# Kernel optimization log

Measured on AMD Instinct MI355X. Metric: run time of the kernel, lower is better.

Reference implementation:

```python
import jax, jax.numpy as jnp
import numpy as np

EMBED_DIM = 1024
NUM_HEADS = 16
HEAD_DIM = EMBED_DIM // NUM_HEADS
B, SQ, SKV = 2, 2048, 2048


def setup_inputs() -> dict:
    key = jax.random.key(0)
    ks = jax.random.split(key, 12)
    s = 1.0 / np.sqrt(EMBED_DIM)
    inp = {
        "query": jax.random.normal(ks[0], (B, SQ, EMBED_DIM), jnp.float32),
        "key": jax.random.normal(ks[1], (B, SKV, EMBED_DIM), jnp.float32),
        "value": jax.random.normal(ks[2], (B, SKV, EMBED_DIM), jnp.float32),
        "Wq": jax.random.normal(ks[3], (EMBED_DIM, EMBED_DIM), jnp.float32) * s,
        "bq": jnp.zeros((EMBED_DIM,), jnp.float32),
        "Wk": jax.random.normal(ks[4], (EMBED_DIM, EMBED_DIM), jnp.float32) * s,
        "bk": jnp.zeros((EMBED_DIM,), jnp.float32),
        "Wv": jax.random.normal(ks[5], (EMBED_DIM, EMBED_DIM), jnp.float32) * s,
        "bv": jnp.zeros((EMBED_DIM,), jnp.float32),
        "Wo": jax.random.normal(ks[6], (EMBED_DIM, EMBED_DIM), jnp.float32) * s,
        "bo": jnp.zeros((EMBED_DIM,), jnp.float32),
        "ln_gamma": jnp.ones((EMBED_DIM,), jnp.float32),
        "ln_beta": jnp.zeros((EMBED_DIM,), jnp.float32),
    }
    return inp


def reference(query, key, value, Wq, bq, Wk, bk, Wv, bv, Wo, bo, ln_gamma, ln_beta):
    b, sq, d = query.shape
    skv = key.shape[1]
    residual = query
    # projections -> [b, h, s, hd]
    Q = (query @ Wq + bq).reshape(b, sq, NUM_HEADS, HEAD_DIM).transpose(0, 2, 1, 3)
    K = (key @ Wk + bk).reshape(b, skv, NUM_HEADS, HEAD_DIM).transpose(0, 2, 1, 3)
    V = (value @ Wv + bv).reshape(b, skv, NUM_HEADS, HEAD_DIM).transpose(0, 2, 1, 3)
    scores = jnp.einsum("bhqd,bhkd->bhqk", Q, K) / jnp.sqrt(jnp.float32(HEAD_DIM)).astype(Q.dtype)
    attn = jax.nn.softmax(scores, axis=-1)  # dropout identity in eval
    attended = jnp.einsum("bhqk,bhkd->bhqd", attn, V)
    attended = attended.transpose(0, 2, 1, 3).reshape(b, sq, d)
    out = attended @ Wo + bo
    x = out + residual
    mu = jnp.mean(x, axis=-1, keepdims=True)
    var = jnp.var(x, axis=-1, keepdims=True)
    return (x - mu) / jnp.sqrt(var + 1e-5) * ln_gamma + ln_beta
```

## Files before the change

### kernel.cpp

```cpp
#include <hip/hip_runtime.h>

#define EMBED 1024
#define NHEAD 16
#define HDIM  64
#define BATCH 2
#define SEQ   2048
#define ROWS  (BATCH*SEQ)

typedef __bf16 bf16x8 __attribute__((ext_vector_type(8)));
typedef float  f32x4  __attribute__((ext_vector_type(4)));
typedef float  f32x16 __attribute__((ext_vector_type(16)));
typedef unsigned short u16x8 __attribute__((ext_vector_type(8)));
typedef unsigned short u16x4 __attribute__((ext_vector_type(4)));
typedef unsigned int   u32x2 __attribute__((ext_vector_type(2)));

__device__ __forceinline__ unsigned short f2bf(float f) {
    unsigned int u = __float_as_uint(f);
    u += 0x7FFFu + ((u >> 16) & 1u);
    return (unsigned short)(u >> 16);
}
__device__ __forceinline__ f32x4 zero4() { f32x4 z = {0.f, 0.f, 0.f, 0.f}; return z; }

__device__ __forceinline__ unsigned int cvtpk_bf16(float lo, float hi) {
    unsigned int r;
    asm("v_cvt_pk_bf16_f32 %0, %1, %2" : "=v"(r) : "v"(lo), "v"(hi));
    return r;
}
__device__ __forceinline__ void pl32swap(unsigned int &a, unsigned int &b) {
    asm("v_permlane32_swap_b32 %0, %1" : "+v"(a), "+v"(b));
}
__device__ __forceinline__ float exp2_hw(float x) {
    float r;
    asm("v_exp_f32 %0, %1" : "=v"(r) : "v"(x));
    return r;
}

__device__ __forceinline__ void gl_lds16(const unsigned short* g, unsigned short* l) {
    __builtin_amdgcn_global_load_lds(
        (const __attribute__((address_space(1))) void*)g,
        (__attribute__((address_space(3))) void*)l, 16, 0, 0);
}

__global__ __launch_bounds__(256) void cvt3_kernel(const float* __restrict__ q,
                                                   const float* __restrict__ k,
                                                   const float* __restrict__ v,
                                                   unsigned short* __restrict__ qo,
                                                   unsigned short* __restrict__ ko,
                                                   unsigned short* __restrict__ vo) {
    const float* in; unsigned short* out;
    if (blockIdx.y == 0)      { in = q; out = qo; }
    else if (blockIdx.y == 1) { in = k; out = ko; }
    else                      { in = v; out = vo; }
    int i = (blockIdx.x * 256 + threadIdx.x) * 4;
    float4 vv = *(const float4*)(in + i);
    u16x4 o = {f2bf(vv.x), f2bf(vv.y), f2bf(vv.z), f2bf(vv.w)};
    *(u16x4*)(out + i) = o;
}

__global__ __launch_bounds__(256) void transpose4_kernel(const float* __restrict__ w0,
                                                         const float* __restrict__ w1,
                                                         const float* __restrict__ w2,
                                                         const float* __restrict__ w3,
                                                         unsigned short* __restrict__ o0,
                                                         unsigned short* __restrict__ o1,
                                                         unsigned short* __restrict__ o2,
                                                         unsigned short* __restrict__ o3) {
    const float* in; unsigned short* out;
    if (blockIdx.z == 0)      { in = w0; out = o0; }
    else if (blockIdx.z == 1) { in = w1; out = o1; }
    else if (blockIdx.z == 2) { in = w2; out = o2; }
    else                      { in = w3; out = o3; }
    __shared__ float tile[32][33];
    int tx = threadIdx.x, ty = threadIdx.y;
    int x = blockIdx.x * 32 + tx;
    int y0 = blockIdx.y * 32 + ty;
#pragma unroll
    for (int r = 0; r < 4; ++r)
        tile[ty + 8 * r][tx] = in[(size_t)(y0 + 8 * r) * EMBED + x];
    __syncthreads();
    int ox = blockIdx.y * 32 + tx;
    int oy = blockIdx.x * 32 + ty;
#pragma unroll
    for (int r = 0; r < 4; ++r)
        out[(size_t)(oy + 8 * r) * EMBED + ox] = f2bf(tile[tx][ty + 8 * r]);
}

__global__ __launch_bounds__(256, 2) void gemm_qkv_kernel(
    const unsigned short* __restrict__ qb, const unsigned short* __restrict__ kb,
    const unsigned short* __restrict__ vb,
    const unsigned short* __restrict__ Wqt, const unsigned short* __restrict__ Wkt,
    const unsigned short* __restrict__ Wvt,
    const float* __restrict__ bq, const float* __restrict__ bk, const float* __restrict__ bv,
    unsigned short* __restrict__ Qp, unsigned short* __restrict__ Kp,
    unsigned short* __restrict__ Vtb) {
    __shared__ unsigned short smem[16384];
    const unsigned short *A, *Bt; const float* bias; unsigned short* outp; int mode; float osc;
    if (blockIdx.z == 0)      { A = qb; Bt = Wqt; bias = bq; outp = Qp;  mode = 0; osc = 0.18033688f; }
    else if (blockIdx.z == 1) { A = kb; Bt = Wkt; bias = bk; outp = Kp;  mode = 0; osc = 1.0f; }
    else                      { A = vb; Bt = Wvt; bias = bv; outp = Vtb; mode = 1; osc = 1.0f; }

    const int t = threadIdx.x;
    const int m0 = blockIdx.x * 128, n0 = blockIdx.y * 128;
    const int wave = t >> 6, lane = t & 63;
    const int wr = wave >> 1, wc = wave & 1;
    const int lm = lane & 15, lq = lane >> 4;
    const int sr = t >> 2;
    const int csrc = (t & 3) ^ ((sr >> 1) & 3);
    const int pa = lq ^ ((lm >> 1) & 3);

    const unsigned short* gA = A + (size_t)(m0 + sr) * EMBED + csrc * 8;
    const unsigned short* gB = Bt + (size_t)(n0 + sr) * EMBED + csrc * 8;

    f32x4 acc[4][4];
#pragma unroll
    for (int i = 0; i < 4; ++i)
#pragma unroll
        for (int j = 0; j < 4; ++j) acc[i][j] = zero4();

    gl_lds16(gA,              smem + wave * 512);
    gl_lds16(gA + 64 * EMBED, smem + 2048 + wave * 512);
    gl_lds16(gB,              smem + 8192 + wave * 512);
    gl_lds16(gB + 64 * EMBED, smem + 8192 + 2048 + wave * 512);

    for (int kk = 0; kk < 32; ++kk) {
        __syncthreads();
        if (kk < 31) {
            gA += 32; gB += 32;
            const int nbo = ((kk + 1) & 1) * 4096;
            gl_lds16(gA,              smem + nbo + wave * 512);
            gl_lds16(gA + 64 * EMBED, smem + nbo + 2048 + wave * 512);
            gl_lds16(gB,              smem + 8192 + nbo + wave * 512);
            gl_lds16(gB + 64 * EMBED, smem + 8192 + nbo + 2048 + wave * 512);
        }
        const int cbo = (kk & 1) * 4096;
        bf16x8 af[4], bfr[4];
#pragma unroll
        for (int i = 0; i < 4; ++i)
            af[i] = *(const bf16x8*)&smem[cbo + (wr * 64 + i * 16 + lm) * 32 + pa * 8];
#pragma unroll
        for (int j = 0; j < 4; ++j)
            bfr[j] = *(const bf16x8*)&smem[8192 + cbo + (wc * 64 + j * 16 + lm) * 32 + pa * 8];
#pragma unroll
        for (int i = 0; i < 4; ++i)
#pragma unroll
            for (int j = 0; j < 4; ++j)
                acc[i][j] = __builtin_amdgcn_mfma_f32_16x16x32_bf16(af[i], bfr[j], acc[i][j], 0, 0, 0);
    }

    const int row = t >> 2, seg = t & 3;
    if (mode == 0) {
#pragma unroll
        for (int p = 0; p < 2; ++p) {
            __syncthreads();
            if (wr == p) {
#pragma unroll
                for (int i = 0; i < 4; ++i)
#pragma unroll
                    for (int j = 0; j < 4; ++j) {
                        float bn = bias[n0 + wc * 64 + j * 16 + lm];
                        int nl = wc * 64 + j * 16 + lm;
#pragma unroll
                        for (int r = 0; r < 4; ++r)
                            smem[(i * 16 + lq * 4 + r) * 136 + nl] =
                                f2bf((acc[i][j][r] + bn) * osc);
                    }
            }
            __syncthreads();
            int m = m0 + p * 64 + row;
            int b = m >> 11, sI = m & 2047;
            int ncol = n0 + seg * 32;
            int h = ncol >> 6, hd0 = ncol & 63;
            unsigned short* dst = outp + (((size_t)((b * NHEAD + h) * SEQ + sI)) << 6) + hd0;
            const unsigned short* src = smem + row * 136 + seg * 32;
            *(u16x8*)(dst)      = *(const u16x8*)(src);
            *(u16x8*)(dst + 8)  = *(const u16x8*)(src + 8);
            *(u16x8*)(dst + 16) = *(const u16x8*)(src + 16);
            *(u16x8*)(dst + 24) = *(const u16x8*)(src + 24);
        }
    } else {
#pragma unroll
        for (int p = 0; p < 2; ++p) {
            __syncthreads();
            if (wc == p) {
#pragma unroll
                for (int i = 0; i < 4; ++i)
#pragma unroll
                    for (int j = 0; j < 4; ++j) {
                        float bn = bias[n0 + p * 64 + j * 16 + lm];
                        u16x4 pw = {f2bf(acc[i][j][0] + bn), f2bf(acc[i][j][1] + bn),
                                    f2bf(acc[i][j][2] + bn), f2bf(acc[i][j][3] + bn)};
                        *(u16x4*)&smem[(j * 16 + lm) * 136 + wr * 64 + i * 16 + lq * 4] = pw;
                    }
            }
            __syncthreads();
            int n = n0 + p * 64 + row;
            int h = n >> 6, hd = n & 63;
            int b = m0 >> 11;
            int s0 = (m0 & 2047) + seg * 32;
            unsigned short* dst = outp + ((size_t)((b * NHEAD + h) * HDIM + hd)) * SEQ + s0;
            const unsigned short* src = smem + row * 136 + seg * 32;
            *(u16x8*)(dst)      = *(const u16x8*)(src);
            *(u16x8*)(dst + 8)  = *(const u16x8*)(src + 8);
            *(u16x8*)(dst + 16) = *(const u16x8*)(src + 16);
            *(u16x8*)(dst + 24) = *(const u16x8*)(src + 24);
        }
    }
}

__global__ __launch_bounds__(256, 2) void gemm_o_kernel(
    const unsigned short* __restrict__ att, const unsigned short* __restrict__ Wot,
    const float* __restrict__ bo, float* __restrict__ xbuf,
    const float* __restrict__ residual) {
    __shared__ unsigned short As[2][2048];
    __shared__ unsigned short Bs[2][4096];
    const int t = threadIdx.x;
    const int m0 = blockIdx.x * 64, n0 = blockIdx.y * 128;
    const int wave = t >> 6, lane = t & 63;
    const int lm = lane & 15, lq = lane >> 4;
    const int sr = t >> 2;
    const int csrc = (t & 3) ^ ((sr >> 1) & 3);
    const int pa = lq ^ ((lm >> 1) & 3);

    const unsigned short* gA = att + (size_t)(m0 + sr) * EMBED + csrc * 8;
    const unsigned short* gB = Wot + (size_t)(n0 + sr) * EMBED + csrc * 8;

    f32x4 acc[4][2];
#pragma unroll
    for (int i = 0; i < 4; ++i)
#pragma unroll
        for (int j = 0; j < 2; ++j) acc[i][j] = zero4();

    gl_lds16(gA,              As[0] + wave * 512);
    gl_lds16(gB,              Bs[0] + wave * 512);
    gl_lds16(gB + 64 * EMBED, Bs[0] + 2048 + wave * 512);

    for (int kk = 0; kk < 32; ++kk) {
        __syncthreads();
        if (kk < 31) {
            gA += 32; gB += 32;
            const int nb = (kk + 1) & 1;
            gl_lds16(gA,              As[nb] + wave * 512);
            gl_lds16(gB,              Bs[nb] + wave * 512);
            gl_lds16(gB + 64 * EMBED, Bs[nb] + 2048 + wave * 512);
        }
        const int cb = kk & 1;
        bf16x8 af[4], bfr[2];
#pragma unroll
        for (int i = 0; i < 4; ++i)
            af[i] = *(const bf16x8*)&As[cb][(i * 16 + lm) * 32 + pa * 8];
#pragma unroll
        for (int j = 0; j < 2; ++j)
            bfr[j] = *(const bf16x8*)&Bs[cb][(wave * 32 + j * 16 + lm) * 32 + pa * 8];
#pragma unroll
        for (int i = 0; i < 4; ++i)
#pragma unroll
            for (int j = 0; j < 2; ++j)
                acc[i][j] = __builtin_amdgcn_mfma_f32_16x16x32_bf16(af[i], bfr[j], acc[i][j], 0, 0, 0);
    }

#pragma unroll
    for (int i = 0; i < 4; ++i)
#pragma unroll
        for (int j = 0; j < 2; ++j) {
            int n = n0 + wave * 32 + j * 16 + lm;
            float bn = bo[n];
#pragma unroll
            for (int r = 0; r < 4; ++r) {
                int m = m0 + i * 16 + lq * 4 + r;
                size_t idx = (size_t)m * EMBED + n;
                xbuf[idx] = acc[i][j][r] + bn + residual[idx];
            }
        }
}

__global__ __launch_bounds__(256, 2) void attn_kernel(const unsigned short* __restrict__ Qp,
                                                      const unsigned short* __restrict__ Kp,
                                                      const unsigned short* __restrict__ Vt,
                                                      unsigned short* __restrict__ att) {
    __shared__ unsigned short Ks[16384];
    __shared__ unsigned short Vs[16384];
    const int t = threadIdx.x;
    const int bh = blockIdx.x;
    const int b = bh >> 4, h = bh & 15;
    const int q0 = blockIdx.y * 128;
    const unsigned short* Qh = Qp + (size_t)bh * SEQ * HDIM;
    const unsigned short* Kh = Kp + (size_t)bh * SEQ * HDIM;
    const unsigned short* Vh = Vt + (size_t)bh * HDIM * SEQ;
    const int wave = t >> 6, lane = t & 63;
    const int ln31 = lane & 31, half = lane >> 5;

    bf16x8 qf[4];
    {
        const unsigned short* qptr = Qh + (size_t)(q0 + wave * 32 + ln31) * HDIM + half * 8;
#pragma unroll
        for (int s = 0; s < 4; ++s) qf[s] = *(const bf16x8*)(qptr + s * 16);
    }

    const int q8a = t, q8b = 256 + t;
    const int fa = q8a >> 6, fb = q8b >> 6;
    const int ma = q8a & 31, mb = q8b & 31;
    const int ha = (q8a >> 5) & 1, hb = (q8b >> 5) & 1;
    const unsigned short* gK0 = Kh + (size_t)((fa >> 2) * 32 + ma) * HDIM + (fa & 3) * 16 + ha * 8;
    const unsigned short* gK1 = Kh + (size_t)((fb >> 2) * 32 + mb) * HDIM + (fb & 3) * 16 + hb * 8;
    const unsigned short* gV0 = Vh + (size_t)((fa >> 2) * 32 + ma) * SEQ + (fa & 3) * 16 + ha * 8;
    const unsigned short* gV1 = Vh + (size_t)((fb >> 2) * 32 + mb) * SEQ + (fb & 3) * 16 + hb * 8;

    gl_lds16(gK0,              Ks + wave * 512);
    gl_lds16(gK1,              Ks + 2048 + wave * 512);
    gl_lds16(gK0 + 64 * HDIM,  Ks + 4096 + wave * 512);
    gl_lds16(gK1 + 64 * HDIM,  Ks + 4096 + 2048 + wave * 512);
    gl_lds16(gV0,              Vs + wave * 512);
    gl_lds16(gV1,              Vs + 2048 + wave * 512);
    gl_lds16(gV0 + 64,         Vs + 4096 + wave * 512);
    gl_lds16(gV1 + 64,         Vs + 4096 + 2048 + wave * 512);
    gK0 += 128 * HDIM; gK1 += 128 * HDIM; gV0 += 128; gV1 += 128;
    gl_lds16(gK0,              Ks + 8192 + wave * 512);
    gl_lds16(gK1,              Ks + 8192 + 2048 + wave * 512);
    gl_lds16(gK0 + 64 * HDIM,  Ks + 8192 + 4096 + wave * 512);
    gl_lds16(gK1 + 64 * HDIM,  Ks + 8192 + 4096 + 2048 + wave * 512);
    gl_lds16(gV0,              Vs + 8192 + wave * 512);
    gl_lds16(gV1,              Vs + 8192 + 2048 + wave * 512);
    gl_lds16(gV0 + 64,         Vs + 8192 + 4096 + wave * 512);
    gl_lds16(gV1 + 64,         Vs + 8192 + 4096 + 2048 + wave * 512);
    gK0 += 128 * HDIM; gK1 += 128 * HDIM; gV0 += 128; gV1 += 128;

    f32x16 Oacc[2];
#pragma unroll
    for (int mo = 0; mo < 2; ++mo)
#pragma unroll
        for (int r = 0; r < 16; ++r) Oacc[mo][r] = 0.f;
    float l_run = 0.f;

    for (int kt2 = 0; kt2 < 16; ++kt2) {
        if (kt2 < 15) { asm volatile("s_waitcnt vmcnt(8)" ::: "memory"); }
        else          { asm volatile("s_waitcnt vmcnt(0)" ::: "memory"); }
        __builtin_amdgcn_s_barrier();
        const int cbo = (kt2 & 1) * 8192;

        f32x16 S[2][2];
#pragma unroll
        for (int tl = 0; tl < 2; ++tl)
#pragma unroll
            for (int mt = 0; mt < 2; ++mt)
#pragma unroll
                for (int r = 0; r < 16; ++r) S[tl][mt][r] = -17.312340f;

        __builtin_amdgcn_s_setprio(1);
#pragma unroll
        for (int tl = 0; tl < 2; ++tl)
#pragma unroll
            for (int mt = 0; mt < 2; ++mt) {
#pragma unroll
                for (int s = 0; s < 4; ++s) {
                    bf16x8 af = *(const bf16x8*)&Ks[cbo + tl * 4096 + (mt * 4 + s) * 512 + half * 256 + ln31 * 8];
                    S[tl][mt] = __builtin_amdgcn_mfma_f32_32x32x16_bf16(af, qf[s], S[tl][mt], 0, 0, 0);
                }
            }
        __builtin_amdgcn_s_setprio(0);

#pragma unroll
        for (int tl = 0; tl < 2; ++tl) {
            float rp0 = 0.f, rp1 = 0.f, rp2 = 0.f, rp3 = 0.f;
#pragma unroll
            for (int mt = 0; mt < 2; ++mt)
#pragma unroll
                for (int rg = 0; rg < 4; ++rg) {
                    float p0 = exp2_hw(S[tl][mt][rg * 4 + 0]);
                    float p1 = exp2_hw(S[tl][mt][rg * 4 + 1]);
                    float p2 = exp2_hw(S[tl][mt][rg * 4 + 2]);
                    float p3 = exp2_hw(S[tl][mt][rg * 4 + 3]);
                    S[tl][mt][rg * 4 + 0] = p0; rp0 += p0;
                    S[tl][mt][rg * 4 + 1] = p1; rp1 += p1;
                    S[tl][mt][rg * 4 + 2] = p2; rp2 += p2;
                    S[tl][mt][rg * 4 + 3] = p3; rp3 += p3;
                }
            float rs = (rp0 + rp1) + (rp2 + rp3);
            rs += __shfl_xor(rs, 32);
            l_run += rs;

            __builtin_amdgcn_s_setprio(1);
#pragma unroll
            for (int mt = 0; mt < 2; ++mt)
#pragma unroll
                for (int p = 0; p < 2; ++p) {
                    unsigned int a0 = cvtpk_bf16(S[tl][mt][8 * p + 0], S[tl][mt][8 * p + 1]);
                    unsigned int a1 = cvtpk_bf16(S[tl][mt][8 * p + 2], S[tl][mt][8 * p + 3]);
                    unsigned int b0 = cvtpk_bf16(S[tl][mt][8 * p + 4], S[tl][mt][8 * p + 5]);
                    unsigned int b1 = cvtpk_bf16(S[tl][mt][8 * p + 6], S[tl][mt][8 * p + 7]);
                    pl32swap(a0, b0);
                    pl32swap(a1, b1);
                    union { unsigned int u[4]; bf16x8 v; } bp;
                    bp.u[0] = a0; bp.u[1] = a1; bp.u[2] = b0; bp.u[3] = b1;
                    const int sp = mt * 2 + p;
#pragma unroll
                    for (int mo = 0; mo < 2; ++mo) {
                        bf16x8 av = *(const bf16x8*)&Vs[cbo + tl * 4096 + (mo * 4 + sp) * 512 + half * 256 + ln31 * 8];
                        Oacc[mo] = __builtin_amdgcn_mfma_f32_32x32x16_bf16(av, bp.v, Oacc[mo], 0, 0, 0);
                    }
                }
            __builtin_amdgcn_s_setprio(0);
        }

        if (kt2 < 14) {
            __builtin_amdgcn_s_barrier();
            gl_lds16(gK0,              Ks + cbo + wave * 512);
            gl_lds16(gK1,              Ks + cbo + 2048 + wave * 512);
            gl_lds16(gK0 + 64 * HDIM,  Ks + cbo + 4096 + wave * 512);
            gl_lds16(gK1 + 64 * HDIM,  Ks + cbo + 4096 + 2048 + wave * 512);
            gl_lds16(gV0,              Vs + cbo + wave * 512);
            gl_lds16(gV1,              Vs + cbo + 2048 + wave * 512);
            gl_lds16(gV0 + 64,         Vs + cbo + 4096 + wave * 512);
            gl_lds16(gV1 + 64,         Vs + cbo + 4096 + 2048 + wave * 512);
            gK0 += 128 * HDIM; gK1 += 128 * HDIM; gV0 += 128; gV1 += 128;
        }
    }

    float inv = 1.f / l_run;
    int q = q0 + wave * 32 + ln31;
    unsigned short* orow = att + (size_t)(b * SEQ + q) * EMBED + h * HDIM;
#pragma unroll
    for (int mo = 0; mo < 2; ++mo)
#pragma unroll
        for (int rg = 0; rg < 4; ++rg) {
            u16x4 ow = {f2bf(Oacc[mo][rg * 4 + 0] * inv), f2bf(Oacc[mo][rg * 4 + 1] * inv),
                        f2bf(Oacc[mo][rg * 4 + 2] * inv), f2bf(Oacc[mo][rg * 4 + 3] * inv)};
            *(u16x4*)&orow[mo * 32 + rg * 8 + half * 4] = ow;
        }
}

__global__ __launch_bounds__(256) void ln_kernel(const float* __restrict__ x,
                                                 const float* __restrict__ gamma,
                                                 const float* __restrict__ beta,
                                                 float* __restrict__ out) {
    __shared__ float red[8];
    const int row = blockIdx.x, t = threadIdx.x;
    float4 v = *(const float4*)(x + (size_t)row * EMBED + t * 4);
    float s = v.x + v.y + v.z + v.w;
    float ss = v.x * v.x + v.y * v.y + v.z * v.z + v.w * v.w;
#pragma unroll
    for (int o = 1; o < 64; o <<= 1) {
        s += __shfl_xor(s, o);
        ss += __shfl_xor(ss, o);
    }
    int wave = t >> 6, lane = t & 63;
    if (lane == 0) { red[wave] = s; red[4 + wave] = ss; }
    __syncthreads();
    s = red[0] + red[1] + red[2] + red[3];
    ss = red[4] + red[5] + red[6] + red[7];
    float mu = s * (1.f / EMBED);
    float var = ss * (1.f / EMBED) - mu * mu;
    float rstd = rsqrtf(var + 1e-5f);
    float4 g = *(const float4*)(gamma + t * 4);
    float4 bb = *(const float4*)(beta + t * 4);
    float4 o;
    o.x = (v.x - mu) * rstd * g.x + bb.x;
    o.y = (v.y - mu) * rstd * g.y + bb.y;
    o.z = (v.z - mu) * rstd * g.z + bb.z;
    o.w = (v.w - mu) * rstd * g.w + bb.w;
    *(float4*)(out + (size_t)row * EMBED + t * 4) = o;
}

extern "C" void kernel_launch(void* const* d_in, const int* in_sizes, int n_in,
                              void* d_out, int out_size, void* d_ws, size_t ws_size,
                              hipStream_t stream) {
    const float* query = (const float*)d_in[0];
    const float* key_  = (const float*)d_in[1];
    const float* value = (const float*)d_in[2];
    const float* Wq = (const float*)d_in[3];
    const float* bq = (const float*)d_in[4];
    const float* Wk = (const float*)d_in[5];
    const float* bk = (const float*)d_in[6];
    const float* Wv = (const float*)d_in[7];
    const float* bv = (const float*)d_in[8];
    const float* Wo = (const float*)d_in[9];
    const float* bo = (const float*)d_in[10];
    const float* gamma = (const float*)d_in[11];
    const float* beta  = (const float*)d_in[12];

    char* ws = (char*)d_ws;
    const size_t MB = 1024 * 1024;
    unsigned short* qb  = (unsigned short*)(ws + 0);
    unsigned short* kb  = (unsigned short*)(ws + 8 * MB);
    unsigned short* vb  = (unsigned short*)(ws + 16 * MB);
    unsigned short* Wqt = (unsigned short*)(ws + 24 * MB);
    unsigned short* Wkt = (unsigned short*)(ws + 26 * MB);
    unsigned short* Wvt = (unsigned short*)(ws + 28 * MB);
    unsigned short* Wot = (unsigned short*)(ws + 30 * MB);
    unsigned short* Qp  = (unsigned short*)(ws + 32 * MB);
    unsigned short* Kp  = (unsigned short*)(ws + 40 * MB);
    unsigned short* Vtb = (unsigned short*)(ws + 48 * MB);
    unsigned short* att = (unsigned short*)(ws + 0);
    float*          xbuf = (float*)(ws + 8 * MB);

    cvt3_kernel<<<dim3(4096, 3), 256, 0, stream>>>(query, key_, value, qb, kb, vb);
    transpose4_kernel<<<dim3(32, 32, 4), dim3(32, 8), 0, stream>>>(Wq, Wk, Wv, Wo, Wqt, Wkt, Wvt, Wot);

    gemm_qkv_kernel<<<dim3(32, 8, 3), 256, 0, stream>>>(qb, kb, vb, Wqt, Wkt, Wvt,
                                                        bq, bk, bv, Qp, Kp, Vtb);

    attn_kernel<<<dim3(32, 16), 256, 0, stream>>>(Qp, Kp, Vtb, att);

    gemm_o_kernel<<<dim3(64, 8), 256, 0, stream>>>(att, Wot, bo, xbuf, query);
    ln_kernel<<<ROWS, 256, 0, stream>>>(xbuf, gamma, beta, (float*)d_out);
}
```

Baseline: 247.0 us.

## Deepen GEMM prefetch with vmcnt waits and split attention PV accumulators

Both projection GEMM kernels now prefetch two K-slices up front. Each iteration waits with s_waitcnt vmcnt on only the older slice plus a raw barrier, and the refill of a buffer is issued after its compute, so global loads overlap more of the MFMA work than the previous __syncthreads double buffer did. In the attention kernel the PV output accumulator is split into two independent chains per output tile, summed at the end, to break the MFMA accumulation dependency. The cost is more accumulator registers, which may hurt occupancy, and reliance on hand-tuned vmcnt counts being correct.

```diff
diff --git a/kernel.cpp b/kernel.cpp
--- a/kernel.cpp
+++ b/kernel.cpp
@@ -121,17 +121,17 @@
     gl_lds16(gA + 64 * EMBED, smem + 2048 + wave * 512);
     gl_lds16(gB,              smem + 8192 + wave * 512);
     gl_lds16(gB + 64 * EMBED, smem + 8192 + 2048 + wave * 512);
+    gA += 32; gB += 32;
+    gl_lds16(gA,              smem + 4096 + wave * 512);
+    gl_lds16(gA + 64 * EMBED, smem + 4096 + 2048 + wave * 512);
+    gl_lds16(gB,              smem + 8192 + 4096 + wave * 512);
+    gl_lds16(gB + 64 * EMBED, smem + 8192 + 4096 + 2048 + wave * 512);
+    gA += 32; gB += 32;
 
     for (int kk = 0; kk < 32; ++kk) {
-        __syncthreads();
-        if (kk < 31) {
-            gA += 32; gB += 32;
-            const int nbo = ((kk + 1) & 1) * 4096;
-            gl_lds16(gA,              smem + nbo + wave * 512);
-            gl_lds16(gA + 64 * EMBED, smem + nbo + 2048 + wave * 512);
-            gl_lds16(gB,              smem + 8192 + nbo + wave * 512);
-            gl_lds16(gB + 64 * EMBED, smem + 8192 + nbo + 2048 + wave * 512);
-        }
+        if (kk < 31) { asm volatile("s_waitcnt vmcnt(4)" ::: "memory"); }
+        else         { asm volatile("s_waitcnt vmcnt(0)" ::: "memory"); }
+        __builtin_amdgcn_s_barrier();
         const int cbo = (kk & 1) * 4096;
         bf16x8 af[4], bfr[4];
 #pragma unroll
@@ -145,6 +145,14 @@
 #pragma unroll
             for (int j = 0; j < 4; ++j)
                 acc[i][j] = __builtin_amdgcn_mfma_f32_16x16x32_bf16(af[i], bfr[j], acc[i][j], 0, 0, 0);
+        if (kk < 30) {
+            __builtin_amdgcn_s_barrier();
+            gl_lds16(gA,              smem + cbo + wave * 512);
+            gl_lds16(gA + 64 * EMBED, smem + cbo + 2048 + wave * 512);
+            gl_lds16(gB,              smem + 8192 + cbo + wave * 512);
+            gl_lds16(gB + 64 * EMBED, smem + 8192 + cbo + 2048 + wave * 512);
+            gA += 32; gB += 32;
+        }
     }
 
     const int row = t >> 2, seg = t & 3;
@@ -233,16 +241,16 @@
     gl_lds16(gA,              As[0] + wave * 512);
     gl_lds16(gB,              Bs[0] + wave * 512);
     gl_lds16(gB + 64 * EMBED, Bs[0] + 2048 + wave * 512);
+    gA += 32; gB += 32;
+    gl_lds16(gA,              As[1] + wave * 512);
+    gl_lds16(gB,              Bs[1] + wave * 512);
+    gl_lds16(gB + 64 * EMBED, Bs[1] + 2048 + wave * 512);
+    gA += 32; gB += 32;
 
     for (int kk = 0; kk < 32; ++kk) {
-        __syncthreads();
-        if (kk < 31) {
-            gA += 32; gB += 32;
-            const int nb = (kk + 1) & 1;
-            gl_lds16(gA,              As[nb] + wave * 512);
-            gl_lds16(gB,              Bs[nb] + wave * 512);
-            gl_lds16(gB + 64 * EMBED, Bs[nb] + 2048 + wave * 512);
-        }
+        if (kk < 31) { asm volatile("s_waitcnt vmcnt(3)" ::: "memory"); }
+        else         { asm volatile("s_waitcnt vmcnt(0)" ::: "memory"); }
+        __builtin_amdgcn_s_barrier();
         const int cb = kk & 1;
         bf16x8 af[4], bfr[2];
 #pragma unroll
@@ -256,6 +264,13 @@
 #pragma unroll
             for (int j = 0; j < 2; ++j)
                 acc[i][j] = __builtin_amdgcn_mfma_f32_16x16x32_bf16(af[i], bfr[j], acc[i][j], 0, 0, 0);
+        if (kk < 30) {
+            __builtin_amdgcn_s_barrier();
+            gl_lds16(gA,              As[cb] + wave * 512);
+            gl_lds16(gB,              Bs[cb] + wave * 512);
+            gl_lds16(gB + 64 * EMBED, Bs[cb] + 2048 + wave * 512);
+            gA += 32; gB += 32;
+        }
     }
 
 #pragma unroll
@@ -324,11 +339,13 @@
     gl_lds16(gV1 + 64,         Vs + 8192 + 4096 + 2048 + wave * 512);
     gK0 += 128 * HDIM; gK1 += 128 * HDIM; gV0 += 128; gV1 += 128;
 
-    f32x16 Oacc[2];
+    f32x16 Oa[2][2];
 #pragma unroll
     for (int mo = 0; mo < 2; ++mo)
 #pragma unroll
-        for (int r = 0; r < 16; ++r) Oacc[mo][r] = 0.f;
+        for (int pr = 0; pr < 2; ++pr)
+#pragma unroll
+            for (int r = 0; r < 16; ++r) Oa[mo][pr][r] = 0.f;
     float l_run = 0.f;
 
     for (int kt2 = 0; kt2 < 16; ++kt2) {
@@ -395,7 +412,7 @@
 #pragma unroll
                     for (int mo = 0; mo < 2; ++mo) {
                         bf16x8 av = *(const bf16x8*)&Vs[cbo + tl * 4096 + (mo * 4 + sp) * 512 + half * 256 + ln31 * 8];
-                        Oacc[mo] = __builtin_amdgcn_mfma_f32_32x32x16_bf16(av, bp.v, Oacc[mo], 0, 0, 0);
+                        Oa[mo][p] = __builtin_amdgcn_mfma_f32_32x32x16_bf16(av, bp.v, Oa[mo][p], 0, 0, 0);
                     }
                 }
             __builtin_amdgcn_s_setprio(0);
@@ -422,8 +439,10 @@
     for (int mo = 0; mo < 2; ++mo)
 #pragma unroll
         for (int rg = 0; rg < 4; ++rg) {
-            u16x4 ow = {f2bf(Oacc[mo][rg * 4 + 0] * inv), f2bf(Oacc[mo][rg * 4 + 1] * inv),
-                        f2bf(Oacc[mo][rg * 4 + 2] * inv), f2bf(Oacc[mo][rg * 4 + 3] * inv)};
+            u16x4 ow = {f2bf((Oa[mo][0][rg * 4 + 0] + Oa[mo][1][rg * 4 + 0]) * inv),
+                        f2bf((Oa[mo][0][rg * 4 + 1] + Oa[mo][1][rg * 4 + 1]) * inv),
+                        f2bf((Oa[mo][0][rg * 4 + 2] + Oa[mo][1][rg * 4 + 2]) * inv),
+                        f2bf((Oa[mo][0][rg * 4 + 3] + Oa[mo][1][rg * 4 + 3]) * inv)};
             *(u16x4*)&orow[mo * 32 + rg * 8 + half * 4] = ow;
         }
 }
```

Result: faster. 232.2 us (-6.0%).
